# Performance work log

Hardware: AMD Instinct MI355X
Metric: run time of the kernel (lower is better)

Reference implementation:

```python
import jax, jax.numpy as jnp
import numpy as np

B, S, D = 4, 4096, 2048      # batch, seq, model_dim
E = 128                      # emb_dim (hardcoded in module)
H = 128                      # head_dim
TAU = 0.4                    # self.T
BASE = 3.0                   # self.base (gumbel-sigmoid offset)
LN_EPS = 1e-5


def setup_inputs() -> dict:
    key = jax.random.key(0)
    k_x, k_wr, k_wd, k_g = jax.random.split(key, 4)
    x = jax.random.normal(k_x, (B, S, D), dtype=jnp.float32)
    # torch nn.Linear stores weight as [out_features, in_features]
    W_router = jax.random.normal(k_wr, (E, D), dtype=jnp.float32) / np.sqrt(D)
    W_decoder = jax.random.normal(k_wd, (H, E), dtype=jnp.float32) / np.sqrt(E)
    ln_gamma = jnp.ones((E,), dtype=jnp.float32)
    ln_beta = jnp.zeros((E,), dtype=jnp.float32)
    rnn_state = jnp.zeros((E,), dtype=jnp.float32)  # registered buffer, zeros
    # torch: gumbels = -Exp(1).log()  -> standard Gumbel(0,1) noise
    u = jax.random.uniform(k_g, (B, S, H), dtype=jnp.float32, minval=1e-20, maxval=1.0)
    gumbel_noise = -jnp.log(-jnp.log(u))
    return {
        "x": x, "W_router": W_router, "W_decoder": W_decoder,
        "ln_gamma": ln_gamma, "ln_beta": ln_beta, "rnn_state": rnn_state,
        "gumbel_noise": gumbel_noise, "top_k": 32,
    }


def reference(x, W_router, W_decoder, ln_gamma, ln_beta, rnn_state, gumbel_noise, top_k):
    # router linear (no bias): [B,S,D] @ [D,E] -> [B,S,E]
    out = jnp.einsum("bsd,ed->bse", x, W_router)
    full_emb = rnn_state + out
    # LayerNorm over emb dim (biased variance, as torch LayerNorm)
    mu = full_emb.mean(-1, keepdims=True)
    var = full_emb.var(-1, keepdims=True)
    h = (full_emb - mu) / jnp.sqrt(var + LN_EPS) * ln_gamma + ln_beta
    # decoder linear after exact GELU: [B,S,E] @ [E,H] -> [B,S,H]
    logits = jnp.einsum("bse,he->bsh", jax.nn.gelu(h, approximate=False), W_decoder)
    # gumbel-sigmoid (soft): sigmoid((logits + gumbel + offset)/tau)
    binary_approx = jax.nn.sigmoid((logits + gumbel_noise + BASE) / TAU)
    # hard_sample: straight-through round
    binary = jax.lax.stop_gradient(jnp.round(binary_approx) - binary_approx) + binary_approx
    # top-k mask over head_dim
    _, topk_idx = jax.lax.top_k(binary_approx, top_k)            # [B,S,top_k]
    topk_mask = jax.nn.one_hot(topk_idx, H, dtype=binary_approx.dtype).sum(-2)  # [B,S,H]
    cnt = binary.sum(-1, keepdims=True)
    binary = jnp.where(cnt > top_k, topk_mask, binary)
    # fallback: if a token selects nothing, pick argmax of soft scores
    zero_mask = binary.sum(-1, keepdims=True) == 0
    fallback = jax.nn.one_hot(jnp.argmax(binary_approx, axis=-1), H, dtype=binary_approx.dtype)
    binary = jnp.where(zero_mask, fallback, binary)
    binary = binary.reshape(B, S, -1, H)  # [B,S,1,H]
    return binary, binary_approx
```

## Files before the change

kernel.cpp:

```cpp
#include <hip/hip_runtime.h>
#include <math.h>

#define NTOK   16384
#define DDIM   2048
#define EDIM   128
#define HDIM   128
#define TOKT   64
#define KC     64
#define NCH    (DDIM / KC)

typedef __attribute__((ext_vector_type(8))) _Float16 half8;
typedef __attribute__((ext_vector_type(4))) _Float16 half4;
typedef __attribute__((ext_vector_type(4))) float    f32x4;

__device__ __forceinline__ int swz(int t, int e) {
  return t * EDIM + ((e & 96) | ((e ^ t) & 31));
}

__global__ __launch_bounds__(256)
void conv_w(const float* __restrict__ Wr,
            _Float16* __restrict__ wh, _Float16* __restrict__ wl) {
  const int idx  = (int)blockIdx.x * 256 + (int)threadIdx.x;
  const int lane = idx & 63;
  const int ks   = (idx >> 6) & 63;
  const int nt   = idx >> 12;
  const int n    = nt * 16 + (lane & 15);
  const int k0   = ks * 32 + (lane >> 4) * 8;
  half8 h, l;
#pragma unroll
  for (int j = 0; j < 8; ++j) {
    const float w = Wr[(size_t)n * DDIM + k0 + j] * 32.0f;
    const _Float16 hh = (_Float16)w;
    h[j] = hh;
    l[j] = (_Float16)((w - (float)hh) * 2048.0f);
  }
  *(half8*)(wh + (size_t)idx * 8) = h;
  *(half8*)(wl + (size_t)idx * 8) = l;
}

__global__ __launch_bounds__(1024)
void fused_router(const float* __restrict__ x,
                  const _Float16* __restrict__ wsh,
                  const _Float16* __restrict__ wsl,
                  const float* __restrict__ Wd,
                  const float* __restrict__ gamma,
                  const float* __restrict__ beta,
                  const float* __restrict__ rnn,
                  const float* __restrict__ gum,
                  float* __restrict__ outb,
                  float* __restrict__ outa) {
  __shared__ char smraw[65536];
  _Float16* const xh = (_Float16*)smraw;
  _Float16* const xl = xh + 8192;
  float* const A  = (float*)smraw;
  float* const G4 = (float*)(smraw + 32768);

  const int tid  = (int)threadIdx.x;
  const int wv   = __builtin_amdgcn_readfirstlane(tid >> 6);
  const int lane = tid & 63;
  const int t0   = (int)blockIdx.x * TOKT;

  const int mt   = wv & 3;
  const int nt0  = (wv >> 2) * 2;
  const int mrow = lane & 15;
  const int quad = lane >> 4;
  const int tloc = mt * 16 + (lane & 15);

  const int st_t = tid >> 4;
  const int st_k = tid & 15;
  const int wofs = st_t * 64 + (((st_k >> 1) ^ (st_t & 7)) << 3) + ((st_k & 1) << 2);
  const int offA0 = tloc * 64 + (((0 * 4 + quad) ^ (tloc & 7)) << 3);
  const int offA1 = tloc * 64 + (((1 * 4 + quad) ^ (tloc & 7)) << 3);

  f32x4 hh0 = {0,0,0,0}, cr0 = {0,0,0,0}, hh1 = {0,0,0,0}, cr1 = {0,0,0,0};

  const float* xg = x + (size_t)(t0 + st_t) * DDIM + st_k * 4;
  float4 px = *(const float4*)xg;

  {
    half4 hv, lv;
#pragma unroll
    for (int m = 0; m < 4; ++m) {
      const float v = (&px.x)[m];
      const _Float16 h = (_Float16)v;
      hv[m] = h;
      lv[m] = (_Float16)((v - (float)h) * 2048.0f);
    }
    *(half4*)&xh[wofs] = hv;
    *(half4*)&xl[wofs] = lv;
  }

  for (int c = 0; c < NCH; ++c) {
    __syncthreads();
    if (c + 1 < NCH) px = *(const float4*)(xg + (c + 1) * KC);

    const int bo = (c & 1) * 4096;
    const int ks0 = c * 2;
#pragma unroll
    for (int s = 0; s < 2; ++s) {
      const int ks = ks0 + s;
      const half8 ah = *(const half8*)&xh[bo + (s ? offA1 : offA0)];
      const half8 al = *(const half8*)&xl[bo + (s ? offA1 : offA0)];
      const half8 bh0 = *(const half8*)(wsh + ((size_t)((nt0    ) * 64 + ks) * 64 + lane) * 8);
      const half8 bl0 = *(const half8*)(wsl + ((size_t)((nt0    ) * 64 + ks) * 64 + lane) * 8);
      const half8 bh1 = *(const half8*)(wsh + ((size_t)((nt0 + 1) * 64 + ks) * 64 + lane) * 8);
      const half8 bl1 = *(const half8*)(wsl + ((size_t)((nt0 + 1) * 64 + ks) * 64 + lane) * 8);
      hh0 = __builtin_amdgcn_mfma_f32_16x16x32_f16(ah, bh0, hh0, 0, 0, 0);
      cr0 = __builtin_amdgcn_mfma_f32_16x16x32_f16(ah, bl0, cr0, 0, 0, 0);
      cr0 = __builtin_amdgcn_mfma_f32_16x16x32_f16(al, bh0, cr0, 0, 0, 0);
      hh1 = __builtin_amdgcn_mfma_f32_16x16x32_f16(ah, bh1, hh1, 0, 0, 0);
      cr1 = __builtin_amdgcn_mfma_f32_16x16x32_f16(ah, bl1, cr1, 0, 0, 0);
      cr1 = __builtin_amdgcn_mfma_f32_16x16x32_f16(al, bh1, cr1, 0, 0, 0);
    }

    if (c + 1 < NCH) {
      half4 hv, lv;
#pragma unroll
      for (int m = 0; m < 4; ++m) {
        const float v = (&px.x)[m];
        const _Float16 h = (_Float16)v;
        hv[m] = h;
        lv[m] = (_Float16)((v - (float)h) * 2048.0f);
      }
      *(half4*)&xh[((c + 1) & 1) * 4096 + wofs] = hv;
      *(half4*)&xl[((c + 1) & 1) * 4096 + wofs] = lv;
    }
  }

  __syncthreads();
  {
    const int e0e = nt0 * 16 + mrow;
    const int e1e = (nt0 + 1) * 16 + mrow;
    const float r0v = rnn[e0e], r1v = rnn[e1e];
#pragma unroll
    for (int r = 0; r < 4; ++r) {
      const int tt = mt * 16 + quad * 4 + r;
      A[swz(tt, e0e)] = hh0[r] * (1.0f / 32.0f) + cr0[r] * (1.0f / 65536.0f) + r0v;
      A[swz(tt, e1e)] = hh1[r] * (1.0f / 32.0f) + cr1[r] * (1.0f / 65536.0f) + r1v;
    }
  }
  __syncthreads();

  const int e0 = wv * 8;
  {
    const float gm0 = gamma[lane], gm1 = gamma[lane + 64];
    const float bt0 = beta[lane],  bt1 = beta[lane + 64];
    for (int tt = wv * 4; tt < wv * 4 + 4; ++tt) {
      const float v0 = A[swz(tt, lane)];
      const float v1 = A[swz(tt, lane + 64)];
      float s = v0 + v1;
#pragma unroll
      for (int m = 32; m; m >>= 1) s += __shfl_xor(s, m);
      const float mu = s * (1.0f / 128.0f);
      const float d0 = v0 - mu, d1 = v1 - mu;
      float q = d0 * d0 + d1 * d1;
#pragma unroll
      for (int m = 32; m; m >>= 1) q += __shfl_xor(q, m);
      const float rstd = 1.0f / sqrtf(q * (1.0f / 128.0f) + 1e-5f);
      const float h0v = d0 * rstd * gm0 + bt0;
      const float h1v = d1 * rstd * gm1 + bt1;
      const float g0 = 0.5f * h0v * (1.0f + erff(h0v * 0.70710678118654752f));
      const float g1 = 0.5f * h1v * (1.0f + erff(h1v * 0.70710678118654752f));
      const int e0a = lane, e1a = lane + 64;
      G4[(tt * 32 + (((e0a >> 2) ^ (tt & 31)))) * 4 + (e0a & 3)] = g0;
      G4[(tt * 32 + (((e1a >> 2) ^ (tt & 31)))) * 4 + (e1a & 3)] = g1;
    }
  }
  __syncthreads();

  {
    float acc2[8];
#pragma unroll
    for (int j = 0; j < 8; ++j) acc2[j] = 0.0f;
    const float4* wd4 = (const float4*)(Wd + (size_t)e0 * EDIM);
#pragma unroll 2
    for (int kg = 0; kg < EDIM / 4; ++kg) {
      const float4 gv = *(const float4*)&G4[(lane * 32 + (kg ^ (lane & 31))) * 4];
#pragma unroll
      for (int j = 0; j < 8; ++j) {
        const float4 w = wd4[(size_t)j * (EDIM / 4) + kg];
        acc2[j] = fmaf(gv.x, w.x,
                  fmaf(gv.y, w.y,
                  fmaf(gv.z, w.z,
                  fmaf(gv.w, w.w, acc2[j]))));
      }
    }
    __syncthreads();
#pragma unroll
    for (int j = 0; j < 8; ++j) A[swz(lane, e0 + j)] = acc2[j];
  }
  __syncthreads();

  for (int tt = wv * 4; tt < wv * 4 + 4; ++tt) {
    const size_t T = (size_t)(t0 + tt);
    const float l0 = A[swz(tt, lane)];
    const float l1 = A[swz(tt, lane + 64)];
    const float gn0 = gum[T * HDIM + lane];
    const float gn1 = gum[T * HDIM + lane + 64];
    const float z0 = (l0 + gn0 + 3.0f) * 2.5f;
    const float z1 = (l1 + gn1 + 3.0f) * 2.5f;
    const float ba0 = 1.0f / (1.0f + expf(-z0));
    const float ba1 = 1.0f / (1.0f + expf(-z1));
    const unsigned ub0 = __float_as_uint(ba0);
    const unsigned ub1 = __float_as_uint(ba1);
    const int r0 = ba0 > 0.5f;
    const int r1 = ba1 > 0.5f;
    const int cnt = __popcll(__ballot(r0)) + __popcll(__ballot(r1));
    float bin0, bin1;
    if (cnt > 32) {
      unsigned v = 0u;
#pragma unroll
      for (int b = 29; b >= 0; --b) {
        const unsigned cand = v | (1u << b);
        const int cc = __popcll(__ballot(ub0 >= cand)) + __popcll(__ballot(ub1 >= cand));
        if (cc >= 32) v = cand;
      }
      const int cgt = __popcll(__ballot(ub0 > v)) + __popcll(__ballot(ub1 > v));
      const int r = 32 - cgt;
      const unsigned long long t0b = __ballot(ub0 == v);
      const unsigned long long t1b = __ballot(ub1 == v);
      const int n0 = __popcll(t0b);
      const unsigned long long mlt = (1ull << lane) - 1ull;
      const int rk0 = __popcll(t0b & mlt);
      const int rk1 = n0 + __popcll(t1b & mlt);
      bin0 = (ub0 > v || (ub0 == v && rk0 < r)) ? 1.0f : 0.0f;
      bin1 = (ub1 > v || (ub1 == v && rk1 < r)) ? 1.0f : 0.0f;
    } else if (cnt == 0) {
      float m = fmaxf(ba0, ba1);
#pragma unroll
      for (int mm = 32; mm; mm >>= 1) m = fmaxf(m, __shfl_xor(m, mm));
      const unsigned long long e0b = __ballot(ba0 == m);
      const unsigned long long e1b = __ballot(ba1 == m);
      const int hstar = e0b ? (__ffsll((unsigned long long)e0b) - 1)
                            : (64 + __ffsll((unsigned long long)e1b) - 1);
      bin0 = (lane == hstar) ? 1.0f : 0.0f;
      bin1 = (lane + 64 == hstar) ? 1.0f : 0.0f;
    } else {
      bin0 = r0 ? 1.0f : 0.0f;
      bin1 = r1 ? 1.0f : 0.0f;
    }
    outb[T * HDIM + lane]      = bin0;
    outb[T * HDIM + lane + 64] = bin1;
    outa[T * HDIM + lane]      = ba0;
    outa[T * HDIM + lane + 64] = ba1;
  }
}

extern "C" void kernel_launch(void* const* d_in, const int* in_sizes, int n_in,
                              void* d_out, int out_size, void* d_ws, size_t ws_size,
                              hipStream_t stream) {
  (void)in_sizes; (void)n_in; (void)ws_size; (void)out_size;
  const float* x   = (const float*)d_in[0];
  const float* Wr  = (const float*)d_in[1];
  const float* Wd  = (const float*)d_in[2];
  const float* gm  = (const float*)d_in[3];
  const float* bt  = (const float*)d_in[4];
  const float* rnn = (const float*)d_in[5];
  const float* gum = (const float*)d_in[6];
  float* outb = (float*)d_out;
  float* outa = outb + (size_t)NTOK * HDIM;

  _Float16* wh = (_Float16*)d_ws;
  _Float16* wl = wh + (size_t)EDIM * DDIM;

  conv_w<<<dim3(128), dim3(256), 0, stream>>>(Wr, wh, wl);
  fused_router<<<dim3(NTOK / TOKT), dim3(1024), 0, stream>>>(
      x, wh, wl, Wd, gm, bt, rnn, gum, outb, outa);
}
```

Before: 262.4 us.

## Stage router weights in LDS and swap wave tiling to share B fragments

The router GEMM main loop now stages both x and the pre-split fp16 hi/lo weight tiles through double-buffered shared memory. Previously each wave loaded weights directly from global memory. Waves are re-mapped so each owns one output column tile and two token tiles, and the K chunk is halved to 32 to fit the extra buffer. Dedicated thread groups load x (first 4 waves) and weights (waves 8-15). This reduces redundant global weight traffic, at the cost of twice as many barrier-separated iterations.

```diff
diff --git a/kernel.cpp b/kernel.cpp
--- a/kernel.cpp
+++ b/kernel.cpp
@@ -6,11 +6,10 @@
 #define EDIM   128
 #define HDIM   128
 #define TOKT   64
-#define KC     64
+#define KC     32
 #define NCH    (DDIM / KC)
 
 typedef __attribute__((ext_vector_type(8))) _Float16 half8;
-typedef __attribute__((ext_vector_type(4))) _Float16 half4;
 typedef __attribute__((ext_vector_type(4))) float    f32x4;
 
 __device__ __forceinline__ int swz(int t, int e) {
@@ -50,8 +49,7 @@
                   float* __restrict__ outb,
                   float* __restrict__ outa) {
   __shared__ char smraw[65536];
-  _Float16* const xh = (_Float16*)smraw;
-  _Float16* const xl = xh + 8192;
+  _Float16* const xs = (_Float16*)smraw;
   float* const A  = (float*)smraw;
   float* const G4 = (float*)(smraw + 32768);
 
@@ -60,83 +58,120 @@
   const int lane = tid & 63;
   const int t0   = (int)blockIdx.x * TOKT;
 
-  const int mt   = wv & 3;
-  const int nt0  = (wv >> 2) * 2;
-  const int mrow = lane & 15;
+  const int nt   = wv & 7;
+  const int mt0  = (wv >> 3) * 2;
+  const int mt1  = mt0 + 1;
   const int quad = lane >> 4;
-  const int tloc = mt * 16 + (lane & 15);
-
-  const int st_t = tid >> 4;
-  const int st_k = tid & 15;
-  const int wofs = st_t * 64 + (((st_k >> 1) ^ (st_t & 7)) << 3) + ((st_k & 1) << 2);
-  const int offA0 = tloc * 64 + (((0 * 4 + quad) ^ (tloc & 7)) << 3);
-  const int offA1 = tloc * 64 + (((1 * 4 + quad) ^ (tloc & 7)) << 3);
+  const int col  = lane & 15;
+
+  const int offA0 = (mt0 * 64 + lane) * 8;
+  const int offA1 = (mt1 * 64 + lane) * 8;
+  const int offB  = 8192 + nt * 1024 + lane * 8;
+
+  const bool xstage = tid < 256;
+  const int  sx_t   = tid >> 2;
+  const int  sx_kq  = tid & 3;
+  const float* xg   = x + (size_t)(t0 + sx_t) * DDIM + sx_kq * 8;
+  const int  sx_off = ((sx_t >> 4) * 64 + sx_kq * 16 + (sx_t & 15)) * 8;
+
+  const bool wstage = wv >= 8;
+  const int  ntw    = wv & 7;
+  const _Float16* whg = wsh + (size_t)ntw * 32768 + (size_t)lane * 8;
+  const _Float16* wlg = wsl + (size_t)ntw * 32768 + (size_t)lane * 8;
+  const int  sw_off = 8192 + ntw * 1024 + lane * 8;
 
   f32x4 hh0 = {0,0,0,0}, cr0 = {0,0,0,0}, hh1 = {0,0,0,0}, cr1 = {0,0,0,0};
 
-  const float* xg = x + (size_t)(t0 + st_t) * DDIM + st_k * 4;
-  float4 px = *(const float4*)xg;
-
-  {
-    half4 hv, lv;
+  if (xstage) {
+    const float4 a = *(const float4*)xg;
+    const float4 bq = *(const float4*)(xg + 4);
+    half8 h, l;
 #pragma unroll
     for (int m = 0; m < 4; ++m) {
-      const float v = (&px.x)[m];
-      const _Float16 h = (_Float16)v;
-      hv[m] = h;
-      lv[m] = (_Float16)((v - (float)h) * 2048.0f);
-    }
-    *(half4*)&xh[wofs] = hv;
-    *(half4*)&xl[wofs] = lv;
-  }
-
+      const float v = (&a.x)[m];
+      const _Float16 hv = (_Float16)v;
+      h[m] = hv; l[m] = (_Float16)((v - (float)hv) * 2048.0f);
+    }
+#pragma unroll
+    for (int m = 0; m < 4; ++m) {
+      const float v = (&bq.x)[m];
+      const _Float16 hv = (_Float16)v;
+      h[m + 4] = hv; l[m + 4] = (_Float16)((v - (float)hv) * 2048.0f);
+    }
+    *(half8*)&xs[sx_off] = h;
+    *(half8*)&xs[2048 + sx_off] = l;
+  }
+  if (wstage) {
+    const half8 h = *(const half8*)whg;
+    const half8 l = *(const half8*)wlg;
+    *(half8*)&xs[sw_off] = h;
+    *(half8*)&xs[sw_off + 512] = l;
+  }
+
+  float4 pxa, pxb; half8 pwh, pwl;
   for (int c = 0; c < NCH; ++c) {
     __syncthreads();
-    if (c + 1 < NCH) px = *(const float4*)(xg + (c + 1) * KC);
-
-    const int bo = (c & 1) * 4096;
-    const int ks0 = c * 2;
-#pragma unroll
-    for (int s = 0; s < 2; ++s) {
-      const int ks = ks0 + s;
-      const half8 ah = *(const half8*)&xh[bo + (s ? offA1 : offA0)];
-      const half8 al = *(const half8*)&xl[bo + (s ? offA1 : offA0)];
-      const half8 bh0 = *(const half8*)(wsh + ((size_t)((nt0    ) * 64 + ks) * 64 + lane) * 8);
-      const half8 bl0 = *(const half8*)(wsl + ((size_t)((nt0    ) * 64 + ks) * 64 + lane) * 8);
-      const half8 bh1 = *(const half8*)(wsh + ((size_t)((nt0 + 1) * 64 + ks) * 64 + lane) * 8);
-      const half8 bl1 = *(const half8*)(wsl + ((size_t)((nt0 + 1) * 64 + ks) * 64 + lane) * 8);
-      hh0 = __builtin_amdgcn_mfma_f32_16x16x32_f16(ah, bh0, hh0, 0, 0, 0);
-      cr0 = __builtin_amdgcn_mfma_f32_16x16x32_f16(ah, bl0, cr0, 0, 0, 0);
-      cr0 = __builtin_amdgcn_mfma_f32_16x16x32_f16(al, bh0, cr0, 0, 0, 0);
-      hh1 = __builtin_amdgcn_mfma_f32_16x16x32_f16(ah, bh1, hh1, 0, 0, 0);
-      cr1 = __builtin_amdgcn_mfma_f32_16x16x32_f16(ah, bl1, cr1, 0, 0, 0);
-      cr1 = __builtin_amdgcn_mfma_f32_16x16x32_f16(al, bh1, cr1, 0, 0, 0);
-    }
-
+    const int b  = c & 1;
+    const int bn = b ^ 1;
     if (c + 1 < NCH) {
-      half4 hv, lv;
-#pragma unroll
-      for (int m = 0; m < 4; ++m) {
-        const float v = (&px.x)[m];
-        const _Float16 h = (_Float16)v;
-        hv[m] = h;
-        lv[m] = (_Float16)((v - (float)h) * 2048.0f);
-      }
-      *(half4*)&xh[((c + 1) & 1) * 4096 + wofs] = hv;
-      *(half4*)&xl[((c + 1) & 1) * 4096 + wofs] = lv;
-    }
-  }
-
+      if (xstage) {
+        pxa = *(const float4*)(xg + (c + 1) * KC);
+        pxb = *(const float4*)(xg + (c + 1) * KC + 4);
+      }
+      if (wstage) {
+        pwh = *(const half8*)(whg + (size_t)(c + 1) * 512);
+        pwl = *(const half8*)(wlg + (size_t)(c + 1) * 512);
+      }
+    }
+    const half8 ah0 = *(const half8*)&xs[b * 4096 + offA0];
+    const half8 al0 = *(const half8*)&xs[b * 4096 + 2048 + offA0];
+    const half8 ah1 = *(const half8*)&xs[b * 4096 + offA1];
+    const half8 al1 = *(const half8*)&xs[b * 4096 + 2048 + offA1];
+    const half8 bh  = *(const half8*)&xs[b * 8192 + offB];
+    const half8 bl  = *(const half8*)&xs[b * 8192 + offB + 512];
+
+    hh0 = __builtin_amdgcn_mfma_f32_16x16x32_f16(ah0, bh, hh0, 0, 0, 0);
+    cr0 = __builtin_amdgcn_mfma_f32_16x16x32_f16(ah0, bl, cr0, 0, 0, 0);
+    cr0 = __builtin_amdgcn_mfma_f32_16x16x32_f16(al0, bh, cr0, 0, 0, 0);
+    hh1 = __builtin_amdgcn_mfma_f32_16x16x32_f16(ah1, bh, hh1, 0, 0, 0);
+    cr1 = __builtin_amdgcn_mfma_f32_16x16x32_f16(ah1, bl, cr1, 0, 0, 0);
+    cr1 = __builtin_amdgcn_mfma_f32_16x16x32_f16(al1, bh, cr1, 0, 0, 0);
+
+    if (c + 1 < NCH) {
+      if (xstage) {
+        half8 h, l;
+#pragma unroll
+        for (int m = 0; m < 4; ++m) {
+          const float v = (&pxa.x)[m];
+          const _Float16 hv = (_Float16)v;
+          h[m] = hv; l[m] = (_Float16)((v - (float)hv) * 2048.0f);
+        }
+#pragma unroll
+        for (int m = 0; m < 4; ++m) {
+          const float v = (&pxb.x)[m];
+          const _Float16 hv = (_Float16)v;
+          h[m + 4] = hv; l[m + 4] = (_Float16)((v - (float)hv) * 2048.0f);
+        }
+        *(half8*)&xs[bn * 4096 + sx_off] = h;
+        *(half8*)&xs[bn * 4096 + 2048 + sx_off] = l;
+      }
+      if (wstage) {
+        *(half8*)&xs[bn * 8192 + sw_off] = pwh;
+        *(half8*)&xs[bn * 8192 + sw_off + 512] = pwl;
+      }
+    }
+  }
   __syncthreads();
+
   {
-    const int e0e = nt0 * 16 + mrow;
-    const int e1e = (nt0 + 1) * 16 + mrow;
-    const float r0v = rnn[e0e], r1v = rnn[e1e];
+    const int e  = nt * 16 + col;
+    const float rv = rnn[e];
 #pragma unroll
     for (int r = 0; r < 4; ++r) {
-      const int tt = mt * 16 + quad * 4 + r;
-      A[swz(tt, e0e)] = hh0[r] * (1.0f / 32.0f) + cr0[r] * (1.0f / 65536.0f) + r0v;
-      A[swz(tt, e1e)] = hh1[r] * (1.0f / 32.0f) + cr1[r] * (1.0f / 65536.0f) + r1v;
+      A[swz(mt0 * 16 + quad * 4 + r, e)] =
+          hh0[r] * (1.0f / 32.0f) + cr0[r] * (1.0f / 65536.0f) + rv;
+      A[swz(mt1 * 16 + quad * 4 + r, e)] =
+          hh1[r] * (1.0f / 32.0f) + cr1[r] * (1.0f / 65536.0f) + rv;
     }
   }
   __syncthreads();
```

After: 259.7 us. Within noise of the previous version (-1.1%).
